# Kernel optimization log

Measured on AMD Instinct MI355X. Metric: run time of the kernel, lower is better.

The kernel has to match this reference:

```python
import jax, jax.numpy as jnp
import numpy as np

L, B, S, D = 12, 2, 2048, 768
QK, H, V = 128, 512, 32000
SCALE = 128 ** (-0.5)


def setup_inputs() -> dict:
    key = jax.random.key(0)
    ks = jax.random.split(key, 11)
    p = lambda k, shp: jax.random.normal(k, shp, dtype=jnp.float32) * 0.02
    return {
        "layer_outputs": jax.random.normal(ks[0], (L, B, S, D), dtype=jnp.float32),
        "Wq": p(ks[1], (D, QK)), "bq": jnp.zeros((QK,), jnp.float32),
        "Wk": p(ks[2], (D, QK)), "bk": jnp.zeros((QK,), jnp.float32),
        "Wv": p(ks[3], (D, H)),  "bv": jnp.zeros((H,), jnp.float32),
        "W1": p(ks[4], (H, H // 2)), "b1": jnp.zeros((H // 2,), jnp.float32),
        "W2": p(ks[5], (H // 2, V)), "b2": jnp.zeros((V,), jnp.float32),
    }


def reference(layer_outputs, Wq, bq, Wk, bk, Wv, bv, W1, b1, W2, b2):
    # layer_outputs: (L, B, S, D) -> h: (S, L, B, D) as in torch permute(2,0,1,3)
    h = jnp.transpose(layer_outputs, (2, 0, 1, 3))
    q_in = h.mean(axis=1)                              # (S, B, D)
    q = jax.nn.relu(q_in @ Wq + bq)                    # (S, B, 128)
    k = jax.nn.relu(h @ Wk + bk)                       # (S, L, B, 128)
    scores = jnp.einsum('sbd,slbd->slb', q, k)[..., None] * SCALE  # (S, L, B, 1)
    attn = jax.nn.softmax(scores, axis=1)              # softmax over layer axis
    v = h @ Wv + bv                                    # (S, L, B, H)
    agg = jnp.sum(attn * v, axis=1)                    # (S, B, H)
    agg = jnp.transpose(agg, (1, 0, 2))                # (B, S, H)
    mid = jax.nn.relu(agg @ W1 + b1)                   # (B, S, H//2); dropout is eval-mode identity
    return mid @ W2 + b2                               # (B, S, V)
```

## Files before the change

### kernel.cpp

```cpp
#include <hip/hip_runtime.h>

#define Snum 2048
#define SCALE 0.08838834764831845f

typedef __attribute__((ext_vector_type(8))) __bf16 bf16x8;
typedef __attribute__((ext_vector_type(4))) float f32x4;

__device__ inline unsigned short f2bf(float f) {
    unsigned int u = __float_as_uint(f);
    unsigned int r = u + 0x7FFFu + ((u >> 16) & 1u);
    return (unsigned short)(r >> 16);
}
__device__ inline float bf2f(unsigned short u) {
    return __uint_as_float(((unsigned)u) << 16);
}
__device__ inline void gld_lds16(const unsigned short* g, unsigned short* l) {
    __builtin_amdgcn_global_load_lds(
        (const __attribute__((address_space(1))) unsigned int*)g,
        (__attribute__((address_space(3))) unsigned int*)l, 16, 0, 0);
}

__global__ __launch_bounds__(256) void prep_all(
    const float* __restrict__ Wk, const float* __restrict__ Wq,
    unsigned short* __restrict__ Wqkt,
    const float* __restrict__ Wv,
    const float* __restrict__ W1,
    const float* __restrict__ bv, const float* __restrict__ b1,
    unsigned short* __restrict__ Gtb,
    float* __restrict__ bp)
{
    const int id = blockIdx.x;
    const int tid = threadIdx.x;

    if (id < 192) {
        __shared__ float t[32][33];
        const int q = (id < 96) ? id : (id - 96);
        const float* in = (id < 96) ? Wk : Wq;
        unsigned short* out = Wqkt + (id < 96 ? 0 : (size_t)128 * 768);
        const int bx = q & 3, by = q >> 2;
        const int tx = tid & 31, ty = tid >> 5;
        #pragma unroll
        for (int i = 0; i < 4; ++i) {
            int k = by * 32 + ty + i * 8, n = bx * 32 + tx;
            t[ty + i * 8][tx] = in[(size_t)k * 128 + n];
        }
        __syncthreads();
        #pragma unroll
        for (int i = 0; i < 4; ++i) {
            int n = bx * 32 + ty + i * 8, k = by * 32 + tx;
            out[(size_t)n * 768 + k] = f2bf(t[tx][ty + i * 8]);
        }
        return;
    }

    if (id == 288) {
        const int n = tid;
        float s = b1[n];
        for (int h = 0; h < 512; ++h) s += bv[h] * W1[(size_t)h * 256 + n];
        bp[n] = s;
        return;
    }

    __shared__ float wv[8][512];
    const int v0 = (id - 192) * 8;
    for (int i = tid; i < 8 * 512; i += 256) {
        const int v = i >> 9, h = i & 511;
        wv[v][h] = Wv[(size_t)(v0 + v) * 512 + h];
    }
    __syncthreads();

    const int n = tid;
    float acc[8] = {};
    for (int h = 0; h < 512; ++h) {
        const float w1 = W1[(size_t)h * 256 + n];
        #pragma unroll
        for (int v = 0; v < 8; ++v) acc[v] += wv[v][h] * w1;
    }
    unsigned short o[8];
    #pragma unroll
    for (int v = 0; v < 8; ++v) o[v] = f2bf(acc[v]);
    *(ushort4*)&Gtb[(size_t)n * 768 + v0]     = *(ushort4*)&o[0];
    *(ushort4*)&Gtb[(size_t)n * 768 + v0 + 4] = *(ushort4*)&o[4];
}

__global__ __launch_bounds__(256) void proj_qk(
    const float* __restrict__ x, const unsigned short* __restrict__ Bt,
    const float* __restrict__ bk,
    unsigned short* __restrict__ Kall,
    unsigned short* __restrict__ Pq)
{
    __shared__ __align__(16) unsigned short As[2][64 * 32];
    __shared__ __align__(16) unsigned short Bs[2][256 * 32];
    const int tid = threadIdx.x;
    const int wid = tid >> 6, lane = tid & 63;
    const int wn = wid * 64;
    const int lr = lane & 15, g = lane >> 4;
    const int r0 = blockIdx.x * 64;
    const int K = 768, NT = 24;

    const int arow = tid >> 2, akc = (tid & 3) * 8;

    f32x4 acc[4][4] = {};

    float4 a0 = *(const float4*)(x + (size_t)(r0 + arow) * K + akc);
    float4 a1 = *(const float4*)(x + (size_t)(r0 + arow) * K + akc + 4);
    {
        unsigned short v[8];
        v[0] = f2bf(a0.x); v[1] = f2bf(a0.y); v[2] = f2bf(a0.z); v[3] = f2bf(a0.w);
        v[4] = f2bf(a1.x); v[5] = f2bf(a1.y); v[6] = f2bf(a1.z); v[7] = f2bf(a1.w);
        *(uint4*)&As[0][arow * 32 + akc] = *(uint4*)v;
    }
    #pragma unroll
    for (int c = 0; c < 4; ++c) {
        const int rr = wid * 64 + c * 16;
        gld_lds16(Bt + (size_t)(rr + (lane >> 2)) * K + (lane & 3) * 8, &Bs[0][rr * 32]);
    }
    __syncthreads();

    for (int t = 0; t < NT; ++t) {
        const int cur = t & 1, nxt = cur ^ 1;
        if (t + 1 < NT) {
            const int k0 = (t + 1) * 32;
            a0 = *(const float4*)(x + (size_t)(r0 + arow) * K + k0 + akc);
            a1 = *(const float4*)(x + (size_t)(r0 + arow) * K + k0 + akc + 4);
            #pragma unroll
            for (int c = 0; c < 4; ++c) {
                const int rr = wid * 64 + c * 16;
                gld_lds16(Bt + (size_t)(rr + (lane >> 2)) * K + k0 + (lane & 3) * 8,
                          &Bs[nxt][rr * 32]);
            }
        }

        bf16x8 aF[4], bF[4];
        #pragma unroll
        for (int mm = 0; mm < 4; ++mm) aF[mm] = *(const bf16x8*)&As[cur][(mm * 16 + lr) * 32 + g * 8];
        #pragma unroll
        for (int nn = 0; nn < 4; ++nn) bF[nn] = *(const bf16x8*)&Bs[cur][(wn + nn * 16 + lr) * 32 + g * 8];
        #pragma unroll
        for (int mm = 0; mm < 4; ++mm)
            #pragma unroll
            for (int nn = 0; nn < 4; ++nn)
                acc[mm][nn] = __builtin_amdgcn_mfma_f32_16x16x32_bf16(bF[nn], aF[mm], acc[mm][nn], 0, 0, 0);

        if (t + 1 < NT) {
            unsigned short v[8];
            v[0] = f2bf(a0.x); v[1] = f2bf(a0.y); v[2] = f2bf(a0.z); v[3] = f2bf(a0.w);
            v[4] = f2bf(a1.x); v[5] = f2bf(a1.y); v[6] = f2bf(a1.z); v[7] = f2bf(a1.w);
            *(uint4*)&As[nxt][arow * 32 + akc] = *(uint4*)v;
        }
        __syncthreads();
    }

    #pragma unroll
    for (int mm = 0; mm < 4; ++mm)
        #pragma unroll
        for (int nn = 0; nn < 4; ++nn) {
            const int row = r0 + mm * 16 + lr;
            const int colb = wn + nn * 16 + g * 4;
            unsigned short o[4];
            if (colb < 128) {
                #pragma unroll
                for (int reg = 0; reg < 4; ++reg) {
                    float kv = acc[mm][nn][reg] + bk[colb + reg];
                    o[reg] = f2bf(kv > 0.f ? kv : 0.f);
                }
                *(ushort4*)&Kall[(size_t)row * 128 + colb] = *(ushort4*)o;
            } else {
                #pragma unroll
                for (int reg = 0; reg < 4; ++reg) o[reg] = f2bf(acc[mm][nn][reg]);
                *(ushort4*)&Pq[(size_t)row * 128 + (colb - 128)] = *(ushort4*)o;
            }
        }
}

__global__ __launch_bounds__(256) void scores_plus_w2t(
    const float* __restrict__ x,
    const unsigned short* __restrict__ Pq,
    const float* __restrict__ bq,
    const unsigned short* __restrict__ Kall,
    unsigned short* __restrict__ hbar,
    const float* __restrict__ W2, unsigned short* __restrict__ W2t)
{
    if (blockIdx.x >= 1024) {
        __shared__ float t[32][33];
        const int id = blockIdx.x - 1024;
        const int bx = id >> 3, by = id & 7;
        const int tx = threadIdx.x & 31, ty = threadIdx.x >> 5;
        #pragma unroll
        for (int i = 0; i < 4; ++i) {
            int k = by * 32 + ty + i * 8, n = bx * 32 + tx;
            t[ty + i * 8][tx] = W2[(size_t)k * 32000 + n];
        }
        __syncthreads();
        #pragma unroll
        for (int i = 0; i < 4; ++i) {
            int n = bx * 32 + ty + i * 8, k = by * 32 + tx;
            W2t[(size_t)n * 256 + k] = f2bf(t[tx][ty + i * 8]);
        }
        return;
    }

    const int wid = threadIdx.x >> 6, lane = threadIdx.x & 63;
    const int r = blockIdx.x * 4 + wid;
    const int b = r >> 11, s = r & 2047;

    float qa = 0.f, qb_ = 0.f;
    #pragma unroll
    for (int l = 0; l < 12; ++l) {
        const unsigned short* prow = Pq + ((size_t)(l * 2 + b) * Snum + s) * 128 + lane * 2;
        unsigned int u = *(const unsigned int*)prow;
        qa += bf2f((unsigned short)(u & 0xFFFF));
        qb_ += bf2f((unsigned short)(u >> 16));
    }
    float q0 = qa * (1.0f / 12.0f) + bq[lane * 2];
    float q1 = qb_ * (1.0f / 12.0f) + bq[lane * 2 + 1];
    q0 = q0 > 0.f ? q0 : 0.f;
    q1 = q1 > 0.f ? q1 : 0.f;
    q0 = bf2f(f2bf(q0)); q1 = bf2f(f2bf(q1));

    float sc[12];
    #pragma unroll
    for (int l = 0; l < 12; ++l) {
        const unsigned short* krow = Kall + ((size_t)(l * 2 + b) * Snum + s) * 128 + lane * 2;
        unsigned int u = *(const unsigned int*)krow;
        float p = q0 * bf2f((unsigned short)(u & 0xFFFF)) + q1 * bf2f((unsigned short)(u >> 16));
        #pragma unroll
        for (int off = 32; off > 0; off >>= 1) p += __shfl_xor(p, off, 64);
        sc[l] = p * SCALE;
    }
    float m = sc[0];
    #pragma unroll
    for (int l = 1; l < 12; ++l) m = fmaxf(m, sc[l]);
    float att[12], den = 0.f;
    #pragma unroll
    for (int l = 0; l < 12; ++l) { att[l] = __expf(sc[l] - m); den += att[l]; }
    const float inv = 1.0f / den;
    #pragma unroll
    for (int l = 0; l < 12; ++l) att[l] *= inv;

    #pragma unroll
    for (int jv = 0; jv < 3; ++jv) {
        const int d0 = jv * 256 + lane * 4;
        float a0 = 0.f, a1 = 0.f, a2 = 0.f, a3 = 0.f;
        #pragma unroll
        for (int l = 0; l < 12; ++l) {
            const float4 v = *(const float4*)(x + ((size_t)(l * 2 + b) * Snum + s) * 768 + d0);
            a0 += att[l] * v.x; a1 += att[l] * v.y; a2 += att[l] * v.z; a3 += att[l] * v.w;
        }
        ushort4 o;
        o.x = f2bf(a0); o.y = f2bf(a1); o.z = f2bf(a2); o.w = f2bf(a3);
        *(ushort4*)(hbar + (size_t)r * 768 + d0) = o;
    }
}

template <int RELU, int OUT_BF16, int BIAS>
__global__ __launch_bounds__(256) void gemm64(
    const unsigned short* __restrict__ A, const unsigned short* __restrict__ Bt,
    const float* __restrict__ bias, void* __restrict__ out, int M, int N, int K)
{
    __shared__ __align__(16) unsigned short As[2][64 * 32];
    __shared__ __align__(16) unsigned short Bs[2][64 * 32];
    const int tid = threadIdx.x;
    const int bn = blockIdx.x, bm = blockIdx.y;
    const int wid = tid >> 6, lane = tid & 63;
    const int wm = (wid >> 1) * 32, wn = (wid & 1) * 32;
    const int lr = lane & 15, g = lane >> 4;
    const int r0 = bm * 64, c0 = bn * 64;
    const int NT = K / 32;

    const int srow = lane >> 2, skc = (lane & 3) * 8;

    f32x4 acc[2][2] = {};

    gld_lds16(A  + (size_t)(r0 + wid * 16 + srow) * K + skc, &As[0][wid * 16 * 32]);
    gld_lds16(Bt + (size_t)(c0 + wid * 16 + srow) * K + skc, &Bs[0][wid * 16 * 32]);
    __syncthreads();

    for (int t = 0; t < NT; ++t) {
        const int cur = t & 1, nxt = cur ^ 1;
        if (t + 1 < NT) {
            const int k0 = (t + 1) * 32;
            gld_lds16(A  + (size_t)(r0 + wid * 16 + srow) * K + k0 + skc, &As[nxt][wid * 16 * 32]);
            gld_lds16(Bt + (size_t)(c0 + wid * 16 + srow) * K + k0 + skc, &Bs[nxt][wid * 16 * 32]);
        }

        bf16x8 aF[2], bF[2];
        #pragma unroll
        for (int mm = 0; mm < 2; ++mm) aF[mm] = *(const bf16x8*)&As[cur][(wm + mm * 16 + lr) * 32 + g * 8];
        #pragma unroll
        for (int nn = 0; nn < 2; ++nn) bF[nn] = *(const bf16x8*)&Bs[cur][(wn + nn * 16 + lr) * 32 + g * 8];
        #pragma unroll
        for (int mm = 0; mm < 2; ++mm)
            #pragma unroll
            for (int nn = 0; nn < 2; ++nn)
                acc[mm][nn] = __builtin_amdgcn_mfma_f32_16x16x32_bf16(bF[nn], aF[mm], acc[mm][nn], 0, 0, 0);
        __syncthreads();
    }

    #pragma unroll
    for (int mm = 0; mm < 2; ++mm)
        #pragma unroll
        for (int nn = 0; nn < 2; ++nn) {
            const int orow = r0 + wm + mm * 16 + lr;
            const int colb = c0 + wn + nn * 16 + g * 4;
            float vr[4];
            #pragma unroll
            for (int reg = 0; reg < 4; ++reg) {
                float v = acc[mm][nn][reg] + (BIAS ? bias[colb + reg] : 0.f);
                vr[reg] = (RELU && v < 0.f) ? 0.f : v;
            }
            if (OUT_BF16) {
                unsigned short o[4];
                #pragma unroll
                for (int reg = 0; reg < 4; ++reg) o[reg] = f2bf(vr[reg]);
                *(ushort4*)&((unsigned short*)out)[(size_t)orow * N + colb] = *(ushort4*)o;
            } else {
                *(float4*)&((float*)out)[(size_t)orow * N + colb] = *(float4*)vr;
            }
        }
}

__global__ __launch_bounds__(256) void gemm_out(
    const unsigned short* __restrict__ A,
    const unsigned short* __restrict__ Bt,
    const float* __restrict__ bias, float* __restrict__ out)
{
    __shared__ __align__(16) unsigned short As[2][128 * 32];
    __shared__ __align__(16) unsigned short Bs[2][128 * 32];
    const int K = 256, N = 32000, NT = 8;
    const int orig = blockIdx.x;
    const int swz = (orig & 7) * 1000 + (orig >> 3);
    const int bn = swz >> 5, bm = swz & 31;
    const int tid = threadIdx.x;
    const int wid = tid >> 6, lane = tid & 63;
    const int wm = (wid >> 1) * 64, wn = (wid & 1) * 64;
    const int lr = lane & 15, g = lane >> 4;
    const int r0 = bm * 128, c0 = bn * 128;

    f32x4 acc[4][4] = {};

    #pragma unroll
    for (int c = 0; c < 2; ++c) {
        const int rr = wid * 32 + c * 16;
        gld_lds16(A  + (size_t)(r0 + rr + (lane >> 2)) * K + (lane & 3) * 8, &As[0][rr * 32]);
        gld_lds16(Bt + (size_t)(c0 + rr + (lane >> 2)) * K + (lane & 3) * 8, &Bs[0][rr * 32]);
    }
    __syncthreads();

    for (int t = 0; t < NT; ++t) {
        const int cur = t & 1, nxt = cur ^ 1;
        if (t + 1 < NT) {
            const int k0 = (t + 1) * 32;
            #pragma unroll
            for (int c = 0; c < 2; ++c) {
                const int rr = wid * 32 + c * 16;
                gld_lds16(A  + (size_t)(r0 + rr + (lane >> 2)) * K + k0 + (lane & 3) * 8, &As[nxt][rr * 32]);
                gld_lds16(Bt + (size_t)(c0 + rr + (lane >> 2)) * K + k0 + (lane & 3) * 8, &Bs[nxt][rr * 32]);
            }
        }

        bf16x8 aF[4], bF[4];
        #pragma unroll
        for (int mm = 0; mm < 4; ++mm) aF[mm] = *(const bf16x8*)&As[cur][(wm + mm * 16 + lr) * 32 + g * 8];
        #pragma unroll
        for (int nn = 0; nn < 4; ++nn) bF[nn] = *(const bf16x8*)&Bs[cur][(wn + nn * 16 + lr) * 32 + g * 8];
        #pragma unroll
        for (int mm = 0; mm < 4; ++mm)
            #pragma unroll
            for (int nn = 0; nn < 4; ++nn)
                acc[mm][nn] = __builtin_amdgcn_mfma_f32_16x16x32_bf16(bF[nn], aF[mm], acc[mm][nn], 0, 0, 0);
        __syncthreads();
    }

    #pragma unroll
    for (int mm = 0; mm < 4; ++mm)
        #pragma unroll
        for (int nn = 0; nn < 4; ++nn) {
            const int row = r0 + wm + mm * 16 + lr;
            const int colb = c0 + wn + nn * 16 + g * 4;
            const float4 b4 = *(const float4*)&bias[colb];
            f32x4 o = acc[mm][nn];
            o[0] += b4.x; o[1] += b4.y; o[2] += b4.z; o[3] += b4.w;
            __builtin_nontemporal_store(o, (f32x4*)&out[(size_t)row * N + colb]);
        }
}

extern "C" void kernel_launch(void* const* d_in, const int* in_sizes, int n_in,
                              void* d_out, int out_size, void* d_ws, size_t ws_size,
                              hipStream_t stream) {
    (void)in_sizes; (void)n_in; (void)out_size; (void)ws_size;

    const float* x  = (const float*)d_in[0];
    const float* Wq = (const float*)d_in[1];
    const float* bq = (const float*)d_in[2];
    const float* Wk = (const float*)d_in[3];
    const float* bk = (const float*)d_in[4];
    const float* Wv = (const float*)d_in[5];
    const float* bv = (const float*)d_in[6];
    const float* W1 = (const float*)d_in[7];
    const float* b1 = (const float*)d_in[8];
    const float* W2 = (const float*)d_in[9];
    const float* b2 = (const float*)d_in[10];

    char* p = (char*)d_ws;
    unsigned short* Wqkt  = (unsigned short*)p; p += (size_t)256 * 768 * 2;
    unsigned short* Gtb   = (unsigned short*)p; p += (size_t)256 * 768 * 2;
    float*          bprim = (float*)p;          p += (size_t)256 * 4;
    unsigned short* W2t   = (unsigned short*)p; p += (size_t)32000 * 256 * 2;
    unsigned short* Kall  = (unsigned short*)p; p += (size_t)49152 * 128 * 2;
    unsigned short* Pq    = (unsigned short*)p; p += (size_t)49152 * 128 * 2;
    unsigned short* hbar  = (unsigned short*)p; p += (size_t)4096 * 768 * 2;
    unsigned short* midb  = (unsigned short*)p; p += (size_t)4096 * 256 * 2;

    prep_all<<<dim3(289), dim3(256), 0, stream>>>(Wk, Wq, Wqkt, Wv, W1, bv, b1, Gtb, bprim);

    proj_qk<<<dim3(49152 / 64), dim3(256), 0, stream>>>(x, Wqkt, bk, Kall, Pq);

    scores_plus_w2t<<<dim3(1024 + 8000), dim3(256), 0, stream>>>(
        x, Pq, bq, Kall, hbar, W2, W2t);

    gemm64<1, 1, 1><<<dim3(256 / 64, 4096 / 64), dim3(256), 0, stream>>>(
        hbar, Gtb, bprim, midb, 4096, 256, 768);

    gemm_out<<<dim3(8000), dim3(256), 0, stream>>>(midb, W2t, b2, (float*)d_out);
}
```

Before: 284.2 us.

## Process two row tiles per block in output GEMM, overlapping stores with next loads

The output GEMM now has each block compute two consecutive 128-row tiles for the same column tile, halving the grid. The first tile's bias-add and nontemporal stores are issued after the second tile's first loads, with a partial vmcnt wait, so the output writes overlap the next tile's load prologue. Bias values are loaded once per block and reused. The cost is fewer blocks in flight and a hand-written waitcnt that depends on how many memory operations are outstanding.

```diff
diff --git a/kernel.cpp b/kernel.cpp
--- a/kernel.cpp
+++ b/kernel.cpp
@@ -329,60 +329,85 @@
     __shared__ __align__(16) unsigned short Bs[2][128 * 32];
     const int K = 256, N = 32000, NT = 8;
     const int orig = blockIdx.x;
-    const int swz = (orig & 7) * 1000 + (orig >> 3);
-    const int bn = swz >> 5, bm = swz & 31;
+    const int swz = (orig & 7) * 500 + (orig >> 3);
+    const int bn = swz >> 4;
+    const int bp = swz & 15;
     const int tid = threadIdx.x;
     const int wid = tid >> 6, lane = tid & 63;
     const int wm = (wid >> 1) * 64, wn = (wid & 1) * 64;
     const int lr = lane & 15, g = lane >> 4;
-    const int r0 = bm * 128, c0 = bn * 128;
-
-    f32x4 acc[4][4] = {};
-
-    #pragma unroll
-    for (int c = 0; c < 2; ++c) {
-        const int rr = wid * 32 + c * 16;
-        gld_lds16(A  + (size_t)(r0 + rr + (lane >> 2)) * K + (lane & 3) * 8, &As[0][rr * 32]);
-        gld_lds16(Bt + (size_t)(c0 + rr + (lane >> 2)) * K + (lane & 3) * 8, &Bs[0][rr * 32]);
-    }
-    __syncthreads();
-
-    for (int t = 0; t < NT; ++t) {
-        const int cur = t & 1, nxt = cur ^ 1;
-        if (t + 1 < NT) {
-            const int k0 = (t + 1) * 32;
-            #pragma unroll
-            for (int c = 0; c < 2; ++c) {
-                const int rr = wid * 32 + c * 16;
-                gld_lds16(A  + (size_t)(r0 + rr + (lane >> 2)) * K + k0 + (lane & 3) * 8, &As[nxt][rr * 32]);
-                gld_lds16(Bt + (size_t)(c0 + rr + (lane >> 2)) * K + k0 + (lane & 3) * 8, &Bs[nxt][rr * 32]);
+    const int c0 = bn * 128;
+
+    float4 b4[4];
+    #pragma unroll
+    for (int nn = 0; nn < 4; ++nn) b4[nn] = *(const float4*)&bias[c0 + wn + nn * 16 + g * 4];
+
+    f32x4 acc[4][4];
+
+    #define STORE_TILE(R0)                                                        \
+        _Pragma("unroll")                                                         \
+        for (int mm = 0; mm < 4; ++mm) {                                          \
+            _Pragma("unroll")                                                     \
+            for (int nn = 0; nn < 4; ++nn) {                                      \
+                const int row = (R0) + wm + mm * 16 + lr;                         \
+                const int colb = c0 + wn + nn * 16 + g * 4;                       \
+                f32x4 o = acc[mm][nn];                                            \
+                o[0] += b4[nn].x; o[1] += b4[nn].y;                               \
+                o[2] += b4[nn].z; o[3] += b4[nn].w;                               \
+                __builtin_nontemporal_store(o, (f32x4*)&out[(size_t)row * N + colb]); \
+            }                                                                     \
+        }
+
+    for (int half = 0; half < 2; ++half) {
+        const int r0 = bp * 256 + half * 128;
+
+        #pragma unroll
+        for (int c = 0; c < 2; ++c) {
+            const int rr = wid * 32 + c * 16;
+            gld_lds16(A  + (size_t)(r0 + rr + (lane >> 2)) * K + (lane & 3) * 8, &As[0][rr * 32]);
+            gld_lds16(Bt + (size_t)(c0 + rr + (lane >> 2)) * K + (lane & 3) * 8, &Bs[0][rr * 32]);
+        }
+        if (half == 0) {
+            __syncthreads();
+        } else {
+            STORE_TILE(bp * 256)
+            asm volatile("s_waitcnt vmcnt(16)" ::: "memory");
+            __builtin_amdgcn_s_barrier();
+        }
+
+        #pragma unroll
+        for (int mm = 0; mm < 4; ++mm)
+            #pragma unroll
+            for (int nn = 0; nn < 4; ++nn) acc[mm][nn] = (f32x4){0.f, 0.f, 0.f, 0.f};
+
+        for (int t = 0; t < NT; ++t) {
+            const int cur = t & 1, nxt = cur ^ 1;
+            if (t + 1 < NT) {
+                const int k0 = (t + 1) * 32;
+                #pragma unroll
+                for (int c = 0; c < 2; ++c) {
+                    const int rr = wid * 32 + c * 16;
+                    gld_lds16(A  + (size_t)(r0 + rr + (lane >> 2)) * K + k0 + (lane & 3) * 8, &As[nxt][rr * 32]);
+                    gld_lds16(Bt + (size_t)(c0 + rr + (lane >> 2)) * K + k0 + (lane & 3) * 8, &Bs[nxt][rr * 32]);
+                }
             }
-        }
-
-        bf16x8 aF[4], bF[4];
-        #pragma unroll
-        for (int mm = 0; mm < 4; ++mm) aF[mm] = *(const bf16x8*)&As[cur][(wm + mm * 16 + lr) * 32 + g * 8];
-        #pragma unroll
-        for (int nn = 0; nn < 4; ++nn) bF[nn] = *(const bf16x8*)&Bs[cur][(wn + nn * 16 + lr) * 32 + g * 8];
-        #pragma unroll
-        for (int mm = 0; mm < 4; ++mm)
-            #pragma unroll
-            for (int nn = 0; nn < 4; ++nn)
-                acc[mm][nn] = __builtin_amdgcn_mfma_f32_16x16x32_bf16(bF[nn], aF[mm], acc[mm][nn], 0, 0, 0);
-        __syncthreads();
-    }
-
-    #pragma unroll
-    for (int mm = 0; mm < 4; ++mm)
-        #pragma unroll
-        for (int nn = 0; nn < 4; ++nn) {
-            const int row = r0 + wm + mm * 16 + lr;
-            const int colb = c0 + wn + nn * 16 + g * 4;
-            const float4 b4 = *(const float4*)&bias[colb];
-            f32x4 o = acc[mm][nn];
-            o[0] += b4.x; o[1] += b4.y; o[2] += b4.z; o[3] += b4.w;
-            __builtin_nontemporal_store(o, (f32x4*)&out[(size_t)row * N + colb]);
-        }
+
+            bf16x8 aF[4], bF[4];
+            #pragma unroll
+            for (int mm = 0; mm < 4; ++mm) aF[mm] = *(const bf16x8*)&As[cur][(wm + mm * 16 + lr) * 32 + g * 8];
+            #pragma unroll
+            for (int nn = 0; nn < 4; ++nn) bF[nn] = *(const bf16x8*)&Bs[cur][(wn + nn * 16 + lr) * 32 + g * 8];
+            #pragma unroll
+            for (int mm = 0; mm < 4; ++mm)
+                #pragma unroll
+                for (int nn = 0; nn < 4; ++nn)
+                    acc[mm][nn] = __builtin_amdgcn_mfma_f32_16x16x32_bf16(bF[nn], aF[mm], acc[mm][nn], 0, 0, 0);
+            __syncthreads();
+        }
+    }
+
+    STORE_TILE(bp * 256 + 128)
+    #undef STORE_TILE
 }
 
 extern "C" void kernel_launch(void* const* d_in, const int* in_sizes, int n_in,
@@ -422,5 +447,5 @@
     gemm64<1, 1, 1><<<dim3(256 / 64, 4096 / 64), dim3(256), 0, stream>>>(
         hbar, Gtb, bprim, midb, 4096, 256, 768);
 
-    gemm_out<<<dim3(8000), dim3(256), 0, stream>>>(midb, W2t, b2, (float*)d_out);
-}
+    gemm_out<<<dim3(4000), dim3(256), 0, stream>>>(midb, W2t, b2, (float*)d_out);
+}
```

After: 329.4 us. +15.9%, slower.
